# Kernel optimization log

Measured on AMD Instinct MI355X. Metric: run time of the kernel, lower is better.

Reference implementation:

```python
import jax, jax.numpy as jnp
import numpy as np

DIM_Q = 512
DIM_K = 512
DIM_V = 512
NUM_HEADS = 8
TEMPERATURE = 0.1
LN_EPS = 1e-5


def setup_inputs() -> dict:
    key = jax.random.key(0)
    ks = jax.random.split(key, 12)
    B, n_q, n_k = 8, 1024, 1024
    s = 0.02
    return {
        "Q": jax.random.normal(ks[0], (B, n_q, DIM_Q), jnp.float32),
        "K": jax.random.normal(ks[1], (B, n_k, DIM_K), jnp.float32),
        "mask": jnp.ones((B, n_k), dtype=bool),
        "Wq": jax.random.normal(ks[2], (DIM_Q, DIM_V), jnp.float32) * s,
        "bq": jnp.zeros((DIM_V,), jnp.float32),
        "Wk": jax.random.normal(ks[3], (DIM_K, DIM_V), jnp.float32) * s,
        "bk": jnp.zeros((DIM_V,), jnp.float32),
        "Wv": jax.random.normal(ks[4], (DIM_K, DIM_V), jnp.float32) * s,
        "bv": jnp.zeros((DIM_V,), jnp.float32),
        "Wo": jax.random.normal(ks[5], (DIM_V, DIM_V), jnp.float32) * s,
        "bo": jnp.zeros((DIM_V,), jnp.float32),
        "gamma": jnp.ones((DIM_V,), jnp.float32),
        "beta": jnp.zeros((DIM_V,), jnp.float32),
    }


def _mab(Q, K, mask, Wq, bq, Wk, bk, Wv, bv, Wo, bo, gamma, beta):
    B, n_q, _ = Q.shape
    n_k = K.shape[1]
    H = NUM_HEADS
    d_head = DIM_V // H
    # projections, split heads: [B, H, n, d_head]
    Qh = (Q @ Wq + bq).reshape(B, n_q, H, d_head).transpose(0, 2, 1, 3)
    Kh = (K @ Wk + bk).reshape(B, n_k, H, d_head).transpose(0, 2, 1, 3)
    Vh = (K @ Wv + bv).reshape(B, n_k, H, d_head).transpose(0, 2, 1, 3)
    scale = 1.0 / (np.sqrt(d_head) * TEMPERATURE)
    A = jnp.einsum("bhqd,bhkd->bhqk", Qh, Kh) * scale
    A = jnp.where(mask[:, None, None, :], A, -jnp.inf)
    A = jax.nn.softmax(A, axis=-1)
    O = jnp.einsum("bhqk,bhkd->bhqd", A, Vh)
    O = O.transpose(0, 2, 1, 3).reshape(B, n_q, DIM_V)
    # fused output FFN + residual + LN
    O = O + jax.nn.relu(O @ Wo + bo)
    mu = jnp.mean(O, axis=-1, keepdims=True)
    var = jnp.var(O, axis=-1, keepdims=True)
    return (O - mu) * jax.lax.rsqrt(var + LN_EPS) * gamma + beta


def reference(Q, K, mask, Wq, bq, Wk, bk, Wv, bv, Wo, bo, gamma, beta):
    return _mab(Q, K, mask, Wq, bq, Wk, bk, Wv, bv, Wo, bo, gamma, beta)
```

## Files before the change

kernel.cpp:

```cpp
#include <hip/hip_runtime.h>

typedef __bf16 bf16;
typedef bf16 bf16x4 __attribute__((ext_vector_type(4)));
typedef bf16 bf16x8 __attribute__((ext_vector_type(8)));
typedef float floatx4 __attribute__((ext_vector_type(4)));

#define NB 8
#define NQ 1024
#define NK 1024
#define DIM 512
#define NH 8
#define DH 64

__device__ __forceinline__ void async16(const void* g, void* l) {
    __builtin_amdgcn_global_load_lds(
        (const __attribute__((address_space(1))) unsigned int*)(unsigned long long)(g),
        (__attribute__((address_space(3))) unsigned int*)(unsigned long long)(l),
        16, 0, 0);
}

__global__ __launch_bounds__(256) void prep_fused(
    const float* __restrict__ Q, const float* __restrict__ K,
    const float* __restrict__ Wq, const float* __restrict__ Wk,
    const float* __restrict__ Wv, const float* __restrict__ Wo,
    bf16* __restrict__ Qb, bf16* __restrict__ Kb, bf16* __restrict__ Wt)
{
    __shared__ bf16 Tl[64][68];
    const int bid = blockIdx.x;
    if (bid < 4096) {
        const int i = bid * 256 + threadIdx.x;
        float4 a = ((const float4*)Q)[i];
        float4 c = ((const float4*)K)[i];
        bf16x4 qa = {(bf16)a.x, (bf16)a.y, (bf16)a.z, (bf16)a.w};
        bf16x4 ka = {(bf16)c.x, (bf16)c.y, (bf16)c.z, (bf16)c.w};
        *(bf16x4*)(Qb + (size_t)i * 4) = qa;
        *(bf16x4*)(Kb + (size_t)i * 4) = ka;
    } else {
        const int bid2 = bid - 4096;
        const int w = bid2 >> 6;
        const int bx = bid2 & 7, by = (bid2 >> 3) & 7;
        const float* W = (w == 0) ? Wq : (w == 1) ? Wk : (w == 2) ? Wv : Wo;
        bf16* out = Wt + (size_t)w * DIM * DIM;
        const int k0 = bx * 64, n0 = by * 64;
        const int tx = threadIdx.x & 15, ty = threadIdx.x >> 4;
        for (int pass = 0; pass < 4; ++pass) {
            int k = ty + pass * 16;
            float4 v = *(const float4*)&W[(size_t)(k0 + k) * DIM + n0 + tx * 4];
            Tl[tx * 4 + 0][k] = (bf16)v.x;
            Tl[tx * 4 + 1][k] = (bf16)v.y;
            Tl[tx * 4 + 2][k] = (bf16)v.z;
            Tl[tx * 4 + 3][k] = (bf16)v.w;
        }
        __syncthreads();
        for (int pass = 0; pass < 4; ++pass) {
            int n = ty + pass * 16;
            bf16x4 ov = *(const bf16x4*)&Tl[n][tx * 4];
            *(bf16x4*)&out[(size_t)(n0 + n) * DIM + k0 + tx * 4] = ov;
        }
    }
}

__global__ __launch_bounds__(256) void proj_fused(
    const bf16* __restrict__ Qb, const bf16* __restrict__ Kb,
    const bf16* __restrict__ Wt,
    const float* __restrict__ bq, const float* __restrict__ bk,
    const float* __restrict__ bv,
    bf16* __restrict__ Qp, bf16* __restrict__ Kp, bf16* __restrict__ Vpt)
{
    __shared__ __attribute__((aligned(16))) bf16 As[64 * 32];
    __shared__ __attribute__((aligned(16))) bf16 Bs[128 * 32];
    const int t = threadIdx.x;
    const int wave = t >> 6, lane = t & 63, quad = lane >> 4, l16 = lane & 15;
    const int wr = wave >> 1, wc = wave & 1;
    const int bid = blockIdx.x;
    const bool isQ = bid < 512;
    const bf16* A; const bf16* W; int m0, n0;
    if (isQ) { A = Qb; W = Wt;             m0 = (bid >> 2) * 64;  n0 = (bid & 3) * 128; }
    else     { int b2 = bid - 512;
               A = Kb; W = Wt + 512 * DIM; m0 = (b2 >> 3) * 64;   n0 = (b2 & 7) * 128; }

    const bf16* aSrc = A + (size_t)(m0 + (t >> 2)) * DIM + (t & 3) * 8;
    const bf16* wSrc = W + (size_t)(n0 + (t >> 2)) * DIM + (t & 3) * 8;
    bf16* aDst  = As + t * 8;
    bf16* bDst0 = Bs + t * 8;
    bf16* bDst1 = Bs + (t + 256) * 8;

    floatx4 acc[2][4];
    for (int i = 0; i < 2; ++i)
        for (int j = 0; j < 4; ++j) acc[i][j] = (floatx4){0.f, 0.f, 0.f, 0.f};

    for (int kt = 0; kt < 16; ++kt) {
        __syncthreads();
        const int ko = kt * 32;
        async16(aSrc + ko, aDst);
        async16(wSrc + ko, bDst0);
        async16(wSrc + 64 * DIM + ko, bDst1);
        __syncthreads();
        bf16x8 af[2], bfr[4];
        for (int mi = 0; mi < 2; ++mi)
            af[mi] = *(const bf16x8*)(As + (wr * 32 + mi * 16 + l16) * 32 + quad * 8);
        for (int ni = 0; ni < 4; ++ni)
            bfr[ni] = *(const bf16x8*)(Bs + (wc * 64 + ni * 16 + l16) * 32 + quad * 8);
        for (int mi = 0; mi < 2; ++mi)
            for (int ni = 0; ni < 4; ++ni)
                acc[mi][ni] = __builtin_amdgcn_mfma_f32_16x16x32_bf16(
                    af[mi], bfr[ni], acc[mi][ni], 0, 0, 0);
    }

    for (int ni = 0; ni < 4; ++ni) {
        const int n = n0 + wc * 64 + ni * 16 + l16;
        float bb;
        if (isQ) bb = bq[n];
        else     bb = (n < 512) ? bk[n] : bv[n - 512];
        for (int mi = 0; mi < 2; ++mi) {
            for (int r = 0; r < 4; ++r) {
                const int m = m0 + wr * 32 + mi * 16 + quad * 4 + r;
                const float v = acc[mi][ni][r] + bb;
                const int b = m >> 10, q = m & 1023;
                if (isQ) {
                    const int hd = n >> 6, d = n & 63;
                    Qp[((size_t)(b * 8 + hd) * 1024 + q) * 64 + d] = (bf16)v;
                } else if (n < 512) {
                    const int hd = n >> 6, d = n & 63;
                    Kp[((size_t)(b * 8 + hd) * 1024 + q) * 64 + d] = (bf16)v;
                } else {
                    const int nv = n - 512, hd = nv >> 6, d = nv & 63;
                    Vpt[((size_t)(b * 8 + hd) * 64 + d) * 1024 + q] = (bf16)v;
                }
            }
        }
    }
}

__global__ __launch_bounds__(256) void attn_kernel(
    const bf16* __restrict__ Qp, const bf16* __restrict__ Kp,
    const bf16* __restrict__ Vpt, const int* __restrict__ mask,
    bf16* __restrict__ Oa)
{
    const int bh = blockIdx.x & 63, qblk = blockIdx.x >> 6;
    const int b = bh >> 3, hd = bh & 7;
    const int t = threadIdx.x;
    const int wave = t >> 6, lane = t & 63, quad = lane >> 4, l16 = lane & 15;
    const float scale = 1.25f;

    __shared__ __attribute__((aligned(16))) bf16 Kt[64 * 64];
    __shared__ __attribute__((aligned(16))) bf16 Vt[64 * 64];
    __shared__ __attribute__((aligned(16))) bf16 Pl[4][32][72];

    const bf16* Qbase = Qp + ((size_t)bh * NQ + qblk * 128 + wave * 32) * DH;
    const bf16* Kbase = Kp + (size_t)bh * NK * DH;
    const bf16* Vbase = Vpt + (size_t)bh * DH * NK;
    const int* mrow = mask + b * NK;

    bf16x8 qf[2][2];
    for (int g = 0; g < 2; ++g)
        for (int hh = 0; hh < 2; ++hh)
            qf[g][hh] = *(const bf16x8*)(Qbase + (g * 16 + l16) * DH + hh * 32 + quad * 8);

    floatx4 o[2][4];
    float lsum[2][4];
    for (int g = 0; g < 2; ++g)
        for (int i = 0; i < 4; ++i) { o[g][i] = (floatx4){0.f,0.f,0.f,0.f}; lsum[g][i] = 0.f; }

    const int r1 = t >> 3, s1 = t & 7;
    const int p1 = s1 ^ (r1 & 7);
    const bf16* kSrc = Kbase + r1 * 64 + p1 * 8;
    const bf16* vSrc = Vbase + (size_t)r1 * 1024 + p1 * 8;
    bf16* kDst0 = Kt + t * 8;
    bf16* kDst1 = Kt + (t + 256) * 8;
    bf16* vDst0 = Vt + t * 8;
    bf16* vDst1 = Vt + (t + 256) * 8;

    for (int kt = 0; kt < NK / 64; ++kt) {
        __syncthreads();
        async16(kSrc + kt * 4096, kDst0);
        async16(kSrc + kt * 4096 + 32 * 64, kDst1);
        async16(vSrc + kt * 64, vDst0);
        async16(vSrc + kt * 64 + (size_t)32 * 1024, vDst1);
        __syncthreads();

        bf16x8 kb[4][2];
        for (int sub = 0; sub < 4; ++sub) {
            const int rowk = sub * 16 + l16;
            kb[sub][0] = *(const bf16x8*)(Kt + rowk * 64 + ((quad ^ (rowk & 7)) << 3));
            kb[sub][1] = *(const bf16x8*)(Kt + rowk * 64 + (((quad + 4) ^ (rowk & 7)) << 3));
        }
        floatx4 sf[2][4];
        for (int g = 0; g < 2; ++g)
            for (int sub = 0; sub < 4; ++sub) {
                floatx4 s = {0.f, 0.f, 0.f, 0.f};
                s = __builtin_amdgcn_mfma_f32_16x16x32_bf16(qf[g][0], kb[sub][0], s, 0, 0, 0);
                s = __builtin_amdgcn_mfma_f32_16x16x32_bf16(qf[g][1], kb[sub][1], s, 0, 0, 0);
                sf[g][sub] = s;
            }
        for (int sub = 0; sub < 4; ++sub) {
            const int key = kt * 64 + sub * 16 + l16;
            const float madd = (mrow[key] != 0) ? 0.f : -3.0e38f;
            for (int g = 0; g < 2; ++g)
                for (int r = 0; r < 4; ++r) {
                    float p = __expf(sf[g][sub][r] * scale + madd);
                    sf[g][sub][r] = p;
                    lsum[g][r] += p;
                }
        }
        for (int g = 0; g < 2; ++g)
            for (int sub = 0; sub < 4; ++sub)
                for (int r = 0; r < 4; ++r)
                    Pl[wave][g * 16 + quad * 4 + r][sub * 16 + l16] = (bf16)sf[g][sub][r];
        bf16x8 af[2][2];
        for (int g = 0; g < 2; ++g)
            for (int hh = 0; hh < 2; ++hh)
                af[g][hh] = *(const bf16x8*)&Pl[wave][g * 16 + l16][hh * 32 + quad * 8];
        for (int dsub = 0; dsub < 4; ++dsub) {
            const int rowd = dsub * 16 + l16;
            bf16x8 v0 = *(const bf16x8*)(Vt + rowd * 64 + ((quad ^ (rowd & 7)) << 3));
            bf16x8 v1 = *(const bf16x8*)(Vt + rowd * 64 + (((quad + 4) ^ (rowd & 7)) << 3));
            for (int g = 0; g < 2; ++g) {
                o[g][dsub] = __builtin_amdgcn_mfma_f32_16x16x32_bf16(af[g][0], v0, o[g][dsub], 0, 0, 0);
                o[g][dsub] = __builtin_amdgcn_mfma_f32_16x16x32_bf16(af[g][1], v1, o[g][dsub], 0, 0, 0);
            }
        }
    }

    for (int g = 0; g < 2; ++g) {
        float linv[4];
        for (int r = 0; r < 4; ++r) {
            float lr = lsum[g][r];
            lr += __shfl_xor(lr, 1, 64);
            lr += __shfl_xor(lr, 2, 64);
            lr += __shfl_xor(lr, 4, 64);
            lr += __shfl_xor(lr, 8, 64);
            linv[r] = 1.f / lr;
        }
        for (int dsub = 0; dsub < 4; ++dsub) {
            for (int r = 0; r < 4; ++r) {
                const int q = qblk * 128 + wave * 32 + g * 16 + quad * 4 + r;
                const int col = hd * 64 + dsub * 16 + l16;
                Oa[((size_t)(b * NQ + q)) * DIM + col] = (bf16)(o[g][dsub][r] * linv[r]);
            }
        }
    }
}

__global__ __launch_bounds__(256) void ffn_gemm(
    const bf16* __restrict__ Oa, const bf16* __restrict__ W,
    const float* __restrict__ bias, float* __restrict__ Y)
{
    __shared__ __attribute__((aligned(16))) bf16 As[64 * 32];
    __shared__ __attribute__((aligned(16))) bf16 Bs[128 * 32];
    const int t = threadIdx.x;
    const int wave = t >> 6, lane = t & 63, quad = lane >> 4, l16 = lane & 15;
    const int wr = wave >> 1, wc = wave & 1;
    const int m0 = (blockIdx.x >> 2) * 64, n0 = (blockIdx.x & 3) * 128;

    const bf16* aSrc = Oa + (size_t)(m0 + (t >> 2)) * DIM + (t & 3) * 8;
    const bf16* wSrc = W  + (size_t)(n0 + (t >> 2)) * DIM + (t & 3) * 8;
    bf16* aDst  = As + t * 8;
    bf16* bDst0 = Bs + t * 8;
    bf16* bDst1 = Bs + (t + 256) * 8;

    floatx4 acc[2][4];
    for (int i = 0; i < 2; ++i)
        for (int j = 0; j < 4; ++j) acc[i][j] = (floatx4){0.f, 0.f, 0.f, 0.f};

    for (int kt = 0; kt < 16; ++kt) {
        __syncthreads();
        const int ko = kt * 32;
        async16(aSrc + ko, aDst);
        async16(wSrc + ko, bDst0);
        async16(wSrc + 64 * DIM + ko, bDst1);
        __syncthreads();
        bf16x8 af[2], bfr[4];
        for (int mi = 0; mi < 2; ++mi)
            af[mi] = *(const bf16x8*)(As + (wr * 32 + mi * 16 + l16) * 32 + quad * 8);
        for (int ni = 0; ni < 4; ++ni)
            bfr[ni] = *(const bf16x8*)(Bs + (wc * 64 + ni * 16 + l16) * 32 + quad * 8);
        for (int mi = 0; mi < 2; ++mi)
            for (int ni = 0; ni < 4; ++ni)
                acc[mi][ni] = __builtin_amdgcn_mfma_f32_16x16x32_bf16(
                    af[mi], bfr[ni], acc[mi][ni], 0, 0, 0);
    }

    for (int ni = 0; ni < 4; ++ni) {
        const int n = n0 + wc * 64 + ni * 16 + l16;
        const float bb = bias[n];
        for (int mi = 0; mi < 2; ++mi) {
            for (int r = 0; r < 4; ++r) {
                const int m = m0 + wr * 32 + mi * 16 + quad * 4 + r;
                const float ov = (float)Oa[(size_t)m * DIM + n];
                const float v = acc[mi][ni][r] + bb;
                Y[(size_t)m * DIM + n] = ov + fmaxf(v, 0.f);
            }
        }
    }
}

__global__ __launch_bounds__(256) void ln_kernel(
    const float* __restrict__ Y, const float* __restrict__ gamma,
    const float* __restrict__ beta, float* __restrict__ out)
{
    const int row  = blockIdx.x * 4 + (threadIdx.x >> 6);
    const int lane = threadIdx.x & 63;
    const float* y = Y + (size_t)row * DIM;
    float4 a = ((const float4*)y)[lane];
    float4 c = ((const float4*)y)[lane + 64];
    float s  = a.x + a.y + a.z + a.w + c.x + c.y + c.z + c.w;
    float sq = a.x*a.x + a.y*a.y + a.z*a.z + a.w*a.w
             + c.x*c.x + c.y*c.y + c.z*c.z + c.w*c.w;
    for (int mk = 32; mk >= 1; mk >>= 1) {
        s  += __shfl_xor(s,  mk, 64);
        sq += __shfl_xor(sq, mk, 64);
    }
    const float mu  = s * (1.f / 512.f);
    const float var = sq * (1.f / 512.f) - mu * mu;
    const float inv = rsqrtf(var + 1e-5f);
    float4 g1 = ((const float4*)gamma)[lane];
    float4 g2 = ((const float4*)gamma)[lane + 64];
    float4 b1 = ((const float4*)beta)[lane];
    float4 b2 = ((const float4*)beta)[lane + 64];
    float4 o1, o2;
    o1.x = (a.x - mu) * inv * g1.x + b1.x;
    o1.y = (a.y - mu) * inv * g1.y + b1.y;
    o1.z = (a.z - mu) * inv * g1.z + b1.z;
    o1.w = (a.w - mu) * inv * g1.w + b1.w;
    o2.x = (c.x - mu) * inv * g2.x + b2.x;
    o2.y = (c.y - mu) * inv * g2.y + b2.y;
    o2.z = (c.z - mu) * inv * g2.z + b2.z;
    o2.w = (c.w - mu) * inv * g2.w + b2.w;
    float* orow = out + (size_t)row * DIM;
    ((float4*)orow)[lane]      = o1;
    ((float4*)orow)[lane + 64] = o2;
}

extern "C" void kernel_launch(void* const* d_in, const int* in_sizes, int n_in,
                              void* d_out, int out_size, void* d_ws, size_t ws_size,
                              hipStream_t stream) {
    const float* Q  = (const float*)d_in[0];
    const float* K  = (const float*)d_in[1];
    const int*   mask = (const int*)d_in[2];
    const float* Wq = (const float*)d_in[3];
    const float* bq = (const float*)d_in[4];
    const float* Wk = (const float*)d_in[5];
    const float* bk = (const float*)d_in[6];
    const float* Wv = (const float*)d_in[7];
    const float* bv = (const float*)d_in[8];
    const float* Wo = (const float*)d_in[9];
    const float* bo = (const float*)d_in[10];
    const float* gamma = (const float*)d_in[11];
    const float* beta  = (const float*)d_in[12];

    char* ws = (char*)d_ws;
    bf16* Wt  = (bf16*)(ws);
    bf16* Qb  = (bf16*)(ws + 2097152);
    bf16* Kb  = (bf16*)(ws + 10485760);
    bf16* Qp  = (bf16*)(ws + 18874368);
    bf16* Kp  = (bf16*)(ws + 27262976);
    bf16* Vpt = (bf16*)(ws + 35651584);
    bf16* Oa  = (bf16*)(ws + 44040192);
    float* Yf = (float*)(ws + 52428800);
    float* out = (float*)d_out;

    prep_fused<<<4352, 256, 0, stream>>>(Q, K, Wq, Wk, Wv, Wo, Qb, Kb, Wt);
    proj_fused<<<1536, 256, 0, stream>>>(Qb, Kb, Wt, bq, bk, bv, Qp, Kp, Vpt);
    attn_kernel<<<512, 256, 0, stream>>>(Qp, Kp, Vpt, mask, Oa);
    ffn_gemm<<<512, 256, 0, stream>>>(Oa, Wt + 3 * 262144, bo, Yf);
    ln_kernel<<<2048, 256, 0, stream>>>(Yf, gamma, beta, out);
}
```

Before: 202.4 us.

## Enlarge GEMM tiles with swizzled LDS, LDS-staged V transpose, transposed attention scores

The projection GEMM now uses 128x128 tiles with a 64-wide K step and XOR-swizzled LDS, halving the grid. V output is staged through LDS so the transposed layout is written with 16-byte coalesced stores instead of scattered 2-byte stores. The FFN GEMM gets the same 64-wide swizzled K tile. Attention swaps the MFMA operands so each lane holds four consecutive keys, which allows vectorized mask loads, packed P stores and a cheaper row-sum reduction. The larger tiles raise register and LDS use per block, which may lower occupancy.

```diff
diff --git a/kernel.cpp b/kernel.cpp
--- a/kernel.cpp
+++ b/kernel.cpp
@@ -67,67 +67,99 @@
     const float* __restrict__ bv,
     bf16* __restrict__ Qp, bf16* __restrict__ Kp, bf16* __restrict__ Vpt)
 {
-    __shared__ __attribute__((aligned(16))) bf16 As[64 * 32];
-    __shared__ __attribute__((aligned(16))) bf16 Bs[128 * 32];
+    __shared__ __attribute__((aligned(16))) bf16 sh[16384];
+    bf16* As = sh;
+    bf16* Bs = sh + 8192;
     const int t = threadIdx.x;
     const int wave = t >> 6, lane = t & 63, quad = lane >> 4, l16 = lane & 15;
     const int wr = wave >> 1, wc = wave & 1;
     const int bid = blockIdx.x;
-    const bool isQ = bid < 512;
+    const bool isQ = bid < 256;
     const bf16* A; const bf16* W; int m0, n0;
-    if (isQ) { A = Qb; W = Wt;             m0 = (bid >> 2) * 64;  n0 = (bid & 3) * 128; }
-    else     { int b2 = bid - 512;
-               A = Kb; W = Wt + 512 * DIM; m0 = (b2 >> 3) * 64;   n0 = (b2 & 7) * 128; }
-
-    const bf16* aSrc = A + (size_t)(m0 + (t >> 2)) * DIM + (t & 3) * 8;
-    const bf16* wSrc = W + (size_t)(n0 + (t >> 2)) * DIM + (t & 3) * 8;
-    bf16* aDst  = As + t * 8;
-    bf16* bDst0 = Bs + t * 8;
-    bf16* bDst1 = Bs + (t + 256) * 8;
-
-    floatx4 acc[2][4];
-    for (int i = 0; i < 2; ++i)
+    if (isQ) { A = Qb; W = Wt;             m0 = (bid >> 2) * 128;  n0 = (bid & 3) * 128; }
+    else     { int b2 = bid - 256;
+               A = Kb; W = Wt + 512 * DIM; m0 = (b2 >> 3) * 128;   n0 = (b2 & 7) * 128; }
+
+    const int r1 = t >> 3, s1 = t & 7;
+    const int p1 = s1 ^ (r1 & 7);
+    const bf16* aSrc = A + (size_t)(m0 + r1) * DIM + p1 * 8;
+    const bf16* wSrc = W + (size_t)(n0 + r1) * DIM + p1 * 8;
+
+    floatx4 acc[4][4];
+    for (int i = 0; i < 4; ++i)
         for (int j = 0; j < 4; ++j) acc[i][j] = (floatx4){0.f, 0.f, 0.f, 0.f};
 
-    for (int kt = 0; kt < 16; ++kt) {
-        __syncthreads();
-        const int ko = kt * 32;
-        async16(aSrc + ko, aDst);
-        async16(wSrc + ko, bDst0);
-        async16(wSrc + 64 * DIM + ko, bDst1);
-        __syncthreads();
-        bf16x8 af[2], bfr[4];
-        for (int mi = 0; mi < 2; ++mi)
-            af[mi] = *(const bf16x8*)(As + (wr * 32 + mi * 16 + l16) * 32 + quad * 8);
-        for (int ni = 0; ni < 4; ++ni)
-            bfr[ni] = *(const bf16x8*)(Bs + (wc * 64 + ni * 16 + l16) * 32 + quad * 8);
-        for (int mi = 0; mi < 2; ++mi)
-            for (int ni = 0; ni < 4; ++ni)
-                acc[mi][ni] = __builtin_amdgcn_mfma_f32_16x16x32_bf16(
-                    af[mi], bfr[ni], acc[mi][ni], 0, 0, 0);
-    }
-
-    for (int ni = 0; ni < 4; ++ni) {
-        const int n = n0 + wc * 64 + ni * 16 + l16;
-        float bb;
-        if (isQ) bb = bq[n];
-        else     bb = (n < 512) ? bk[n] : bv[n - 512];
-        for (int mi = 0; mi < 2; ++mi) {
-            for (int r = 0; r < 4; ++r) {
-                const int m = m0 + wr * 32 + mi * 16 + quad * 4 + r;
-                const float v = acc[mi][ni][r] + bb;
-                const int b = m >> 10, q = m & 1023;
-                if (isQ) {
-                    const int hd = n >> 6, d = n & 63;
-                    Qp[((size_t)(b * 8 + hd) * 1024 + q) * 64 + d] = (bf16)v;
-                } else if (n < 512) {
-                    const int hd = n >> 6, d = n & 63;
-                    Kp[((size_t)(b * 8 + hd) * 1024 + q) * 64 + d] = (bf16)v;
-                } else {
-                    const int nv = n - 512, hd = nv >> 6, d = nv & 63;
-                    Vpt[((size_t)(b * 8 + hd) * 64 + d) * 1024 + q] = (bf16)v;
+    for (int kt = 0; kt < 8; ++kt) {
+        __syncthreads();
+        const int ko = kt * 64;
+        #pragma unroll
+        for (int j = 0; j < 4; ++j) {
+            async16(aSrc + ko + (size_t)j * 32 * DIM, As + (t + j * 256) * 8);
+            async16(wSrc + ko + (size_t)j * 32 * DIM, Bs + (t + j * 256) * 8);
+        }
+        __syncthreads();
+        #pragma unroll
+        for (int ks = 0; ks < 2; ++ks) {
+            bf16x8 af[4], bfr[4];
+            #pragma unroll
+            for (int mi = 0; mi < 4; ++mi) {
+                const int row = wr * 64 + mi * 16 + l16;
+                af[mi] = *(const bf16x8*)(As + row * 64 + (((ks * 4 + quad) ^ (row & 7)) << 3));
+            }
+            #pragma unroll
+            for (int ni = 0; ni < 4; ++ni) {
+                const int row = wc * 64 + ni * 16 + l16;
+                bfr[ni] = *(const bf16x8*)(Bs + row * 64 + (((ks * 4 + quad) ^ (row & 7)) << 3));
+            }
+            #pragma unroll
+            for (int mi = 0; mi < 4; ++mi)
+                #pragma unroll
+                for (int ni = 0; ni < 4; ++ni)
+                    acc[mi][ni] = __builtin_amdgcn_mfma_f32_16x16x32_bf16(
+                        af[mi], bfr[ni], acc[mi][ni], 0, 0, 0);
+        }
+    }
+
+    const bool isV = (!isQ) && (n0 >= 512);
+    if (!isV) {
+        bf16* out = isQ ? Qp : Kp;
+        const float* bias = isQ ? bq : bk;
+        for (int ni = 0; ni < 4; ++ni) {
+            const int n = n0 + wc * 64 + ni * 16 + l16;
+            const float bb = bias[n];
+            const int hd = n >> 6, d = n & 63;
+            for (int mi = 0; mi < 4; ++mi) {
+                for (int r = 0; r < 4; ++r) {
+                    const int m = m0 + wr * 64 + mi * 16 + quad * 4 + r;
+                    const int b = m >> 10, q = m & 1023;
+                    out[((size_t)(b * 8 + hd) * 1024 + q) * 64 + d] = (bf16)(acc[mi][ni][r] + bb);
                 }
             }
+        }
+    } else {
+        __syncthreads();
+        for (int ni = 0; ni < 4; ++ni) {
+            const int n = wc * 64 + ni * 16 + l16;
+            const float bb = bv[n0 + n - 512];
+            for (int mi = 0; mi < 4; ++mi) {
+                const int mb = wr * 64 + mi * 16 + quad * 4;
+                const int slot = ((mb >> 3) ^ (n & 15));
+                bf16x4 pk = {(bf16)(acc[mi][ni][0] + bb), (bf16)(acc[mi][ni][1] + bb),
+                             (bf16)(acc[mi][ni][2] + bb), (bf16)(acc[mi][ni][3] + bb)};
+                *(bf16x4*)(sh + n * 128 + slot * 8 + (mb & 7)) = pk;
+            }
+        }
+        __syncthreads();
+        const int n = t >> 1, hf = t & 1;
+        const int nv = n0 + n - 512, hd = nv >> 6, d = nv & 63;
+        const int b = m0 >> 10, qb = m0 & 1023;
+        bf16* dst = Vpt + ((size_t)(b * 8 + hd) * 64 + d) * 1024 + qb + hf * 64;
+        #pragma unroll
+        for (int j = 0; j < 8; ++j) {
+            const int ch = hf * 8 + j;
+            const int slot = ch ^ (n & 15);
+            bf16x8 v8 = *(const bf16x8*)(sh + n * 128 + slot * 8);
+            *(bf16x8*)(dst + j * 8) = v8;
         }
     }
 }
@@ -158,9 +190,11 @@
             qf[g][hh] = *(const bf16x8*)(Qbase + (g * 16 + l16) * DH + hh * 32 + quad * 8);
 
     floatx4 o[2][4];
-    float lsum[2][4];
-    for (int g = 0; g < 2; ++g)
-        for (int i = 0; i < 4; ++i) { o[g][i] = (floatx4){0.f,0.f,0.f,0.f}; lsum[g][i] = 0.f; }
+    float lsum[2];
+    for (int g = 0; g < 2; ++g) {
+        lsum[g] = 0.f;
+        for (int i = 0; i < 4; ++i) o[g][i] = (floatx4){0.f, 0.f, 0.f, 0.f};
+    }
 
     const int r1 = t >> 3, s1 = t & 7;
     const int p1 = s1 ^ (r1 & 7);
@@ -180,41 +214,58 @@
         __syncthreads();
 
         bf16x8 kb[4][2];
+        #pragma unroll
         for (int sub = 0; sub < 4; ++sub) {
             const int rowk = sub * 16 + l16;
             kb[sub][0] = *(const bf16x8*)(Kt + rowk * 64 + ((quad ^ (rowk & 7)) << 3));
             kb[sub][1] = *(const bf16x8*)(Kt + rowk * 64 + (((quad + 4) ^ (rowk & 7)) << 3));
         }
         floatx4 sf[2][4];
+        #pragma unroll
         for (int g = 0; g < 2; ++g)
+            #pragma unroll
             for (int sub = 0; sub < 4; ++sub) {
                 floatx4 s = {0.f, 0.f, 0.f, 0.f};
-                s = __builtin_amdgcn_mfma_f32_16x16x32_bf16(qf[g][0], kb[sub][0], s, 0, 0, 0);
-                s = __builtin_amdgcn_mfma_f32_16x16x32_bf16(qf[g][1], kb[sub][1], s, 0, 0, 0);
+                s = __builtin_amdgcn_mfma_f32_16x16x32_bf16(kb[sub][0], qf[g][0], s, 0, 0, 0);
+                s = __builtin_amdgcn_mfma_f32_16x16x32_bf16(kb[sub][1], qf[g][1], s, 0, 0, 0);
                 sf[g][sub] = s;
             }
+        #pragma unroll
         for (int sub = 0; sub < 4; ++sub) {
-            const int key = kt * 64 + sub * 16 + l16;
-            const float madd = (mrow[key] != 0) ? 0.f : -3.0e38f;
-            for (int g = 0; g < 2; ++g)
-                for (int r = 0; r < 4; ++r) {
-                    float p = __expf(sf[g][sub][r] * scale + madd);
-                    sf[g][sub][r] = p;
-                    lsum[g][r] += p;
-                }
-        }
+            const int4 m4 = *(const int4*)&mrow[kt * 64 + sub * 16 + quad * 4];
+            const float md0 = m4.x ? 0.f : -3.0e38f;
+            const float md1 = m4.y ? 0.f : -3.0e38f;
+            const float md2 = m4.z ? 0.f : -3.0e38f;
+            const float md3 = m4.w ? 0.f : -3.0e38f;
+            #pragma unroll
+            for (int g = 0; g < 2; ++g) {
+                float p0 = __expf(sf[g][sub][0] * scale + md0);
+                float p1v = __expf(sf[g][sub][1] * scale + md1);
+                float p2 = __expf(sf[g][sub][2] * scale + md2);
+                float p3 = __expf(sf[g][sub][3] * scale + md3);
+                sf[g][sub][0] = p0; sf[g][sub][1] = p1v;
+                sf[g][sub][2] = p2; sf[g][sub][3] = p3;
+                lsum[g] += p0 + p1v + p2 + p3;
+            }
+        }
+        #pragma unroll
         for (int g = 0; g < 2; ++g)
-            for (int sub = 0; sub < 4; ++sub)
-                for (int r = 0; r < 4; ++r)
-                    Pl[wave][g * 16 + quad * 4 + r][sub * 16 + l16] = (bf16)sf[g][sub][r];
+            #pragma unroll
+            for (int sub = 0; sub < 4; ++sub) {
+                bf16x4 pk = {(bf16)sf[g][sub][0], (bf16)sf[g][sub][1],
+                             (bf16)sf[g][sub][2], (bf16)sf[g][sub][3]};
+                *(bf16x4*)&Pl[wave][g * 16 + l16][sub * 16 + quad * 4] = pk;
+            }
         bf16x8 af[2][2];
         for (int g = 0; g < 2; ++g)
             for (int hh = 0; hh < 2; ++hh)
                 af[g][hh] = *(const bf16x8*)&Pl[wave][g * 16 + l16][hh * 32 + quad * 8];
+        #pragma unroll
         for (int dsub = 0; dsub < 4; ++dsub) {
             const int rowd = dsub * 16 + l16;
             bf16x8 v0 = *(const bf16x8*)(Vt + rowd * 64 + ((quad ^ (rowd & 7)) << 3));
             bf16x8 v1 = *(const bf16x8*)(Vt + rowd * 64 + (((quad + 4) ^ (rowd & 7)) << 3));
+            #pragma unroll
             for (int g = 0; g < 2; ++g) {
                 o[g][dsub] = __builtin_amdgcn_mfma_f32_16x16x32_bf16(af[g][0], v0, o[g][dsub], 0, 0, 0);
                 o[g][dsub] = __builtin_amdgcn_mfma_f32_16x16x32_bf16(af[g][1], v1, o[g][dsub], 0, 0, 0);
@@ -223,15 +274,12 @@
     }
 
     for (int g = 0; g < 2; ++g) {
+        float lr = lsum[g];
+        lr += __shfl_xor(lr, 16, 64);
+        lr += __shfl_xor(lr, 32, 64);
+        const float inv = 1.f / lr;
         float linv[4];
-        for (int r = 0; r < 4; ++r) {
-            float lr = lsum[g][r];
-            lr += __shfl_xor(lr, 1, 64);
-            lr += __shfl_xor(lr, 2, 64);
-            lr += __shfl_xor(lr, 4, 64);
-            lr += __shfl_xor(lr, 8, 64);
-            linv[r] = 1.f / lr;
-        }
+        for (int r = 0; r < 4; ++r) linv[r] = __shfl(inv, quad * 4 + r, 64);
         for (int dsub = 0; dsub < 4; ++dsub) {
             for (int r = 0; r < 4; ++r) {
                 const int q = qblk * 128 + wave * 32 + g * 16 + quad * 4 + r;
@@ -246,39 +294,51 @@
     const bf16* __restrict__ Oa, const bf16* __restrict__ W,
     const float* __restrict__ bias, float* __restrict__ Y)
 {
-    __shared__ __attribute__((aligned(16))) bf16 As[64 * 32];
-    __shared__ __attribute__((aligned(16))) bf16 Bs[128 * 32];
+    __shared__ __attribute__((aligned(16))) bf16 As[64 * 64];
+    __shared__ __attribute__((aligned(16))) bf16 Bs[128 * 64];
     const int t = threadIdx.x;
     const int wave = t >> 6, lane = t & 63, quad = lane >> 4, l16 = lane & 15;
     const int wr = wave >> 1, wc = wave & 1;
     const int m0 = (blockIdx.x >> 2) * 64, n0 = (blockIdx.x & 3) * 128;
 
-    const bf16* aSrc = Oa + (size_t)(m0 + (t >> 2)) * DIM + (t & 3) * 8;
-    const bf16* wSrc = W  + (size_t)(n0 + (t >> 2)) * DIM + (t & 3) * 8;
-    bf16* aDst  = As + t * 8;
-    bf16* bDst0 = Bs + t * 8;
-    bf16* bDst1 = Bs + (t + 256) * 8;
+    const int r1 = t >> 3, s1 = t & 7;
+    const int p1 = s1 ^ (r1 & 7);
+    const bf16* aSrc = Oa + (size_t)(m0 + r1) * DIM + p1 * 8;
+    const bf16* wSrc = W  + (size_t)(n0 + r1) * DIM + p1 * 8;
 
     floatx4 acc[2][4];
     for (int i = 0; i < 2; ++i)
         for (int j = 0; j < 4; ++j) acc[i][j] = (floatx4){0.f, 0.f, 0.f, 0.f};
 
-    for (int kt = 0; kt < 16; ++kt) {
-        __syncthreads();
-        const int ko = kt * 32;
-        async16(aSrc + ko, aDst);
-        async16(wSrc + ko, bDst0);
-        async16(wSrc + 64 * DIM + ko, bDst1);
-        __syncthreads();
-        bf16x8 af[2], bfr[4];
-        for (int mi = 0; mi < 2; ++mi)
-            af[mi] = *(const bf16x8*)(As + (wr * 32 + mi * 16 + l16) * 32 + quad * 8);
-        for (int ni = 0; ni < 4; ++ni)
-            bfr[ni] = *(const bf16x8*)(Bs + (wc * 64 + ni * 16 + l16) * 32 + quad * 8);
-        for (int mi = 0; mi < 2; ++mi)
-            for (int ni = 0; ni < 4; ++ni)
-                acc[mi][ni] = __builtin_amdgcn_mfma_f32_16x16x32_bf16(
-                    af[mi], bfr[ni], acc[mi][ni], 0, 0, 0);
+    for (int kt = 0; kt < 8; ++kt) {
+        __syncthreads();
+        const int ko = kt * 64;
+        async16(aSrc + ko, As + t * 8);
+        async16(aSrc + ko + (size_t)32 * DIM, As + (t + 256) * 8);
+        #pragma unroll
+        for (int j = 0; j < 4; ++j)
+            async16(wSrc + ko + (size_t)j * 32 * DIM, Bs + (t + j * 256) * 8);
+        __syncthreads();
+        #pragma unroll
+        for (int ks = 0; ks < 2; ++ks) {
+            bf16x8 af[2], bfr[4];
+            #pragma unroll
+            for (int mi = 0; mi < 2; ++mi) {
+                const int row = wr * 32 + mi * 16 + l16;
+                af[mi] = *(const bf16x8*)(As + row * 64 + (((ks * 4 + quad) ^ (row & 7)) << 3));
+            }
+            #pragma unroll
+            for (int ni = 0; ni < 4; ++ni) {
+                const int row = wc * 64 + ni * 16 + l16;
+                bfr[ni] = *(const bf16x8*)(Bs + row * 64 + (((ks * 4 + quad) ^ (row & 7)) << 3));
+            }
+            #pragma unroll
+            for (int mi = 0; mi < 2; ++mi)
+                #pragma unroll
+                for (int ni = 0; ni < 4; ++ni)
+                    acc[mi][ni] = __builtin_amdgcn_mfma_f32_16x16x32_bf16(
+                        af[mi], bfr[ni], acc[mi][ni], 0, 0, 0);
+        }
     }
 
     for (int ni = 0; ni < 4; ++ni) {
@@ -361,7 +421,7 @@
     float* out = (float*)d_out;
 
     prep_fused<<<4352, 256, 0, stream>>>(Q, K, Wq, Wk, Wv, Wo, Qb, Kb, Wt);
-    proj_fused<<<1536, 256, 0, stream>>>(Qb, Kb, Wt, bq, bk, bv, Qp, Kp, Vpt);
+    proj_fused<<<768, 256, 0, stream>>>(Qb, Kb, Wt, bq, bk, bv, Qp, Kp, Vpt);
     attn_kernel<<<512, 256, 0, stream>>>(Qp, Kp, Vpt, mask, Oa);
     ffn_gemm<<<512, 256, 0, stream>>>(Oa, Wt + 3 * 262144, bo, Yf);
     ln_kernel<<<2048, 256, 0, stream>>>(Yf, gamma, beta, out);
```

Result: faster. 189.9 us (-6.2%).
